# Optimization experiments

Hardware: AMD Instinct MI355X
Metric: run time of the kernel (lower is better)

The kernel has to match this reference:

```python
import jax, jax.numpy as jnp
import numpy as np

N, E, DIN, H, DOUT, G = 100000, 1600000, 32, 64, 8, 64
NUM_PROC = 2
EDGE_DIM = 15


def setup_inputs() -> dict:
    key = jax.random.key(0)
    ks = jax.random.split(key, 20)
    s = 0.1
    return {
        "x": jax.random.normal(ks[0], (N, DIN), dtype=jnp.float32),
        "edge_index": jax.random.randint(ks[1], (2, E), 0, N, dtype=jnp.int32),
        "edge_attr": jax.random.normal(ks[2], (E, EDGE_DIM), dtype=jnp.float32),
        "batch": jnp.sort(jax.random.randint(ks[3], (N,), 0, G, dtype=jnp.int32)),
        "enc_W": jax.random.normal(ks[4], (DIN, H)) * s,
        "enc_b": jnp.zeros((H,), jnp.float32),
        "lin_W": jax.random.normal(ks[5], (NUM_PROC, H, H)) * s,
        "lin_b": jnp.zeros((NUM_PROC, H), jnp.float32),
        "edge_W": jax.random.normal(ks[6], (NUM_PROC, EDGE_DIM, H)) * s,
        "edge_b": jnp.zeros((NUM_PROC, H), jnp.float32),
        "att_W1": jax.random.normal(ks[7], (H, H // 2)) * s,
        "att_b1": jnp.zeros((H // 2,), jnp.float32),
        "att_W2": jax.random.normal(ks[8], (H // 2, 1)) * s,
        "att_b2": jnp.zeros((1,), jnp.float32),
        "dec_W1": jax.random.normal(ks[9], (H, H // 2)) * s,
        "dec_b1": jnp.zeros((H // 2,), jnp.float32),
        "dec_W2": jax.random.normal(ks[10], (H // 2, DOUT)) * s,
        "dec_b2": jnp.zeros((DOUT,), jnp.float32),
    }


def reference(x, edge_index, edge_attr, batch, enc_W, enc_b, lin_W, lin_b,
              edge_W, edge_b, att_W1, att_b1, att_W2, att_b2,
              dec_W1, dec_b1, dec_W2, dec_b2):
    src, dst = edge_index[0], edge_index[1]
    n = x.shape[0]
    # encoder
    h = jax.nn.relu(x @ enc_W + enc_b)
    # message passing layers: gather x_j -> linear + edge embedding -> scatter-add
    for l in range(NUM_PROC):
        msg = h[src] @ lin_W[l] + lin_b[l] + edge_attr @ edge_W[l] + edge_b[l]  # [E, H]
        h = jax.nn.relu(jax.ops.segment_sum(msg, dst, num_segments=n))
    # attention global pooling: segment softmax over graphs in `batch`
    scores = (jax.nn.relu(h @ att_W1 + att_b1) @ att_W2 + att_b2)[:, 0]  # [N]
    m = jax.ops.segment_max(scores, batch, num_segments=G)
    e = jnp.exp(scores - m[batch])
    denom = jax.ops.segment_sum(e, batch, num_segments=G)
    attn = e / denom[batch]
    g = jax.ops.segment_sum(h * attn[:, None], batch, num_segments=G)  # [G, H]
    # decoder
    return jax.nn.relu(g @ dec_W1 + dec_b1) @ dec_W2 + dec_b2
```

## Files before the change

### kernel.cpp

```cpp
#include <hip/hip_runtime.h>

#define DIN 32
#define HDIM 64
#define DOUT 8
#define NGRAPH 64
#define EDIM 15
#define SCAN_BS 512

__device__ __forceinline__ int clampidx(int v, int n) {
    return ((unsigned)v < (unsigned)n) ? v : 0;
}

__device__ __forceinline__ unsigned short f2b(float f) {
    unsigned int u = __float_as_uint(f);
    u = (u + 0x7FFF + ((u >> 16) & 1)) >> 16;
    return (unsigned short)u;
}
__device__ __forceinline__ float b2f(unsigned short b) {
    return __uint_as_float(((unsigned int)b) << 16);
}

__device__ __forceinline__ unsigned int fkey(float f) {
    unsigned int b = __float_as_uint(f);
    return (b & 0x80000000u) ? ~b : (b | 0x80000000u);
}
__device__ __forceinline__ float funkey(unsigned int k) {
    unsigned int b = (k & 0x80000000u) ? (k ^ 0x80000000u) : ~k;
    return __uint_as_float(b);
}

__global__ __launch_bounds__(256) void k_enc_b(const float* __restrict__ x,
                                               const float* __restrict__ W,
                                               const float* __restrict__ b,
                                               unsigned short* __restrict__ h, int n_nodes) {
    __shared__ float xs[4][DIN];
    const int j = threadIdx.x & 63;
    const int q = threadIdx.x >> 6;
    const int n = blockIdx.x * 4 + q;
    const bool ok = (n < n_nodes);
    if (ok && j < DIN) xs[q][j] = x[(size_t)n * DIN + j];
    __syncthreads();
    if (ok) {
        float acc = b[j];
#pragma unroll
        for (int k = 0; k < DIN; ++k) acc = fmaf(xs[q][k], W[k * HDIM + j], acc);
        h[(size_t)n * HDIM + j] = f2b(fmaxf(acc, 0.f));
    }
}

__global__ __launch_bounds__(256) void k_ecvt(const float* __restrict__ eattr,
                                              unsigned short* __restrict__ eb, int E) {
    size_t i = (size_t)blockIdx.x * blockDim.x + threadIdx.x;
    const size_t stride = (size_t)gridDim.x * blockDim.x;
    const size_t total = (size_t)E * 16;
    for (; i < total; i += stride) {
        int d = (int)(i & 15);
        size_t e = i >> 4;
        eb[i] = (d < EDIM) ? f2b(eattr[e * EDIM + d]) : 0;
    }
}

__global__ __launch_bounds__(256) void k_deg(const int* __restrict__ ei,
                                             int* __restrict__ degi,
                                             int* __restrict__ rank, int E, int n_nodes) {
    int e = blockIdx.x * blockDim.x + threadIdx.x;
    if (e < E) rank[e] = atomicAdd(&degi[clampidx(ei[E + e], n_nodes)], 1);
}

__global__ __launch_bounds__(SCAN_BS) void k_blocksum(const int* __restrict__ degi,
                                                      int* __restrict__ bsum, int n) {
    __shared__ int red[SCAN_BS];
    const int t = threadIdx.x;
    const int i = blockIdx.x * SCAN_BS + t;
    red[t] = (i < n) ? degi[i] : 0;
    __syncthreads();
    for (int off = SCAN_BS / 2; off >= 1; off >>= 1) {
        if (t < off) red[t] += red[t + off];
        __syncthreads();
    }
    if (t == 0) bsum[blockIdx.x] = red[0];
}

__global__ __launch_bounds__(64) void k_bscan(const int* __restrict__ bsum,
                                              int* __restrict__ boff,
                                              int* __restrict__ offsets,
                                              int nblk, int n, int E) {
    if (blockIdx.x == 0 && threadIdx.x == 0) {
        int run = 0;
        for (int b = 0; b < nblk; ++b) { boff[b] = run; run += bsum[b]; }
        offsets[n] = E;
    }
}

__global__ __launch_bounds__(64) void k_fillofs(const int* __restrict__ degi,
                                                const int* __restrict__ boff,
                                                int* __restrict__ offsets, int n) {
    if (threadIdx.x != 0) return;
    const int b = blockIdx.x;
    int run = boff[b];
    const int i0 = b * SCAN_BS;
    const int i1 = (i0 + SCAN_BS < n) ? i0 + SCAN_BS : n;
    for (int i = i0; i < i1; ++i) {
        offsets[i] = run;
        run += degi[i];
    }
}

__global__ __launch_bounds__(256) void k_fill(const int* __restrict__ ei,
                                              const int* __restrict__ offsets,
                                              const int* __restrict__ rank,
                                              int2* __restrict__ pe, int E, int n_nodes) {
    int e = blockIdx.x * blockDim.x + threadIdx.x;
    if (e >= E) return;
    int dst = clampidx(ei[E + e], n_nodes);
    int pos = offsets[dst] + rank[e];
    if ((unsigned)pos < (unsigned)E) pe[pos] = make_int2(clampidx(ei[e], n_nodes), e);
}

__global__ __launch_bounds__(256) void k_gxf0(const unsigned short* __restrict__ hprev,
                                              const unsigned short* __restrict__ eb,
                                              const int* __restrict__ degi,
                                              const int* __restrict__ offsets,
                                              const int2* __restrict__ pe,
                                              const float* __restrict__ linW,
                                              const float* __restrict__ linb,
                                              const float* __restrict__ edgeW,
                                              const float* __restrict__ edgeb,
                                              unsigned short* __restrict__ hnext,
                                              float* __restrict__ ea_out,
                                              int n_nodes, int E) {
    __shared__ float As[4][HDIM];
    __shared__ float es[4][EDIM];
    const int j = threadIdx.x & 63;
    const int q = threadIdx.x >> 6;
    const bool ed = (j < EDIM);
    int w  = (blockIdx.x * blockDim.x + threadIdx.x) >> 6;
    const int nw = (gridDim.x * blockDim.x) >> 6;
    for (int n = w; n < n_nodes; n += nw) {
        int rs = offsets[n], re = offsets[n + 1];
        if (rs < 0) rs = 0;
        if (re > E) re = E;
        if (re < rs) re = rs;
        float A0 = 0.f, A1 = 0.f, A2 = 0.f, A3 = 0.f;
        float e0 = 0.f, e1 = 0.f, e2 = 0.f, e3 = 0.f;
        int jj = rs;
        for (; jj + 4 <= re; jj += 4) {
            int2 p0 = pe[jj], p1 = pe[jj + 1], p2 = pe[jj + 2], p3 = pe[jj + 3];
            int s0 = clampidx(p0.x, n_nodes), s1 = clampidx(p1.x, n_nodes);
            int s2 = clampidx(p2.x, n_nodes), s3 = clampidx(p3.x, n_nodes);
            A0 += b2f(hprev[(size_t)s0 * HDIM + j]);
            A1 += b2f(hprev[(size_t)s1 * HDIM + j]);
            A2 += b2f(hprev[(size_t)s2 * HDIM + j]);
            A3 += b2f(hprev[(size_t)s3 * HDIM + j]);
            if (ed) {
                e0 += b2f(eb[(size_t)clampidx(p0.y, E) * 16 + j]);
                e1 += b2f(eb[(size_t)clampidx(p1.y, E) * 16 + j]);
                e2 += b2f(eb[(size_t)clampidx(p2.y, E) * 16 + j]);
                e3 += b2f(eb[(size_t)clampidx(p3.y, E) * 16 + j]);
            }
        }
        for (; jj < re; ++jj) {
            int2 p = pe[jj];
            A0 += b2f(hprev[(size_t)clampidx(p.x, n_nodes) * HDIM + j]);
            if (ed) e0 += b2f(eb[(size_t)clampidx(p.y, E) * 16 + j]);
        }
        As[q][j] = (A0 + A1) + (A2 + A3);
        float eacc = (e0 + e1) + (e2 + e3);
        if (ed) {
            es[q][j] = eacc;
            ea_out[(size_t)n * 16 + j] = eacc;
        }
        __builtin_amdgcn_wave_barrier();
        float acc = (linb[j] + edgeb[j]) * (float)degi[n];
#pragma unroll
        for (int k = 0; k < HDIM; ++k) acc = fmaf(As[q][k], linW[k * HDIM + j], acc);
#pragma unroll
        for (int k = 0; k < EDIM; ++k) acc = fmaf(es[q][k], edgeW[k * HDIM + j], acc);
        hnext[(size_t)n * HDIM + j] = f2b(fmaxf(acc, 0.f));
    }
}

__global__ __launch_bounds__(256) void k_gxf1(const unsigned short* __restrict__ hprev,
                                              const float* __restrict__ ea,
                                              const int* __restrict__ degi,
                                              const int* __restrict__ offsets,
                                              const int2* __restrict__ pe,
                                              const float* __restrict__ linW,
                                              const float* __restrict__ linb,
                                              const float* __restrict__ edgeW,
                                              const float* __restrict__ edgeb,
                                              float* __restrict__ hnext, int n_nodes, int E) {
    __shared__ float As[4][HDIM];
    __shared__ float es[4][EDIM];
    const int j = threadIdx.x & 63;
    const int q = threadIdx.x >> 6;
    int w  = (blockIdx.x * blockDim.x + threadIdx.x) >> 6;
    const int nw = (gridDim.x * blockDim.x) >> 6;
    for (int n = w; n < n_nodes; n += nw) {
        int rs = offsets[n], re = offsets[n + 1];
        if (rs < 0) rs = 0;
        if (re > E) re = E;
        if (re < rs) re = rs;
        float A0 = 0.f, A1 = 0.f, A2 = 0.f, A3 = 0.f;
        int jj = rs;
        for (; jj + 4 <= re; jj += 4) {
            int s0 = clampidx(pe[jj].x,     n_nodes);
            int s1 = clampidx(pe[jj + 1].x, n_nodes);
            int s2 = clampidx(pe[jj + 2].x, n_nodes);
            int s3 = clampidx(pe[jj + 3].x, n_nodes);
            A0 += b2f(hprev[(size_t)s0 * HDIM + j]);
            A1 += b2f(hprev[(size_t)s1 * HDIM + j]);
            A2 += b2f(hprev[(size_t)s2 * HDIM + j]);
            A3 += b2f(hprev[(size_t)s3 * HDIM + j]);
        }
        for (; jj < re; ++jj) A0 += b2f(hprev[(size_t)clampidx(pe[jj].x, n_nodes) * HDIM + j]);
        As[q][j] = (A0 + A1) + (A2 + A3);
        if (j < EDIM) es[q][j] = ea[(size_t)n * 16 + j];
        __builtin_amdgcn_wave_barrier();
        float acc = (linb[j] + edgeb[j]) * (float)degi[n];
#pragma unroll
        for (int k = 0; k < HDIM; ++k) acc = fmaf(As[q][k], linW[k * HDIM + j], acc);
#pragma unroll
        for (int k = 0; k < EDIM; ++k) acc = fmaf(es[q][k], edgeW[k * HDIM + j], acc);
        hnext[(size_t)n * HDIM + j] = fmaxf(acc, 0.f);
    }
}

__global__ __launch_bounds__(256) void k_sc_b(const float* __restrict__ h,
                                              const float* __restrict__ W1,
                                              const float* __restrict__ b1,
                                              const float* __restrict__ W2,
                                              const float* __restrict__ b2,
                                              float* __restrict__ s, int n_nodes) {
    __shared__ float hs[4][HDIM];
    const int j = threadIdx.x & 63;
    const int q = threadIdx.x >> 6;
    const int n = blockIdx.x * 4 + q;
    const bool ok = (n < n_nodes);
    if (ok) hs[q][j] = h[(size_t)n * HDIM + j];
    __builtin_amdgcn_wave_barrier();
    float t = 0.f;
    if (ok && j < 32) {
        float z = b1[j];
#pragma unroll
        for (int k = 0; k < HDIM; ++k) z = fmaf(hs[q][k], W1[k * 32 + j], z);
        t = fmaxf(z, 0.f) * W2[j];
    }
    t += __shfl_xor(t, 1, 64);
    t += __shfl_xor(t, 2, 64);
    t += __shfl_xor(t, 4, 64);
    t += __shfl_xor(t, 8, 64);
    t += __shfl_xor(t, 16, 64);
    if (ok && j == 0) s[n] = t + b2[0];
}

__global__ __launch_bounds__(256) void k_poolA(const float* __restrict__ s,
                                               const int* __restrict__ batch,
                                               unsigned int* __restrict__ gmaxi, int n_nodes) {
    const int gi = blockIdx.x >> 3;
    const int c  = blockIdx.x & 7;
    __shared__ int se[2];
    __shared__ float red[256];
    if (threadIdx.x == 0) {
        int lo = 0, hi = n_nodes;
        while (lo < hi) { int mid = (lo + hi) >> 1; if (batch[mid] < gi) lo = mid + 1; else hi = mid; }
        se[0] = lo;
        lo = 0; hi = n_nodes;
        while (lo < hi) { int mid = (lo + hi) >> 1; if (batch[mid] < gi + 1) lo = mid + 1; else hi = mid; }
        se[1] = lo;
    }
    __syncthreads();
    const int start = se[0], len = se[1] - se[0];
    const int cs = start + (int)(((long long)len * c) >> 3);
    const int ce = start + (int)(((long long)len * (c + 1)) >> 3);
    float mx = -3.4e38f;
    for (int i = cs + threadIdx.x; i < ce; i += 256) mx = fmaxf(mx, s[i]);
    red[threadIdx.x] = mx;
    __syncthreads();
    for (int off = 128; off >= 1; off >>= 1) {
        if (threadIdx.x < off) red[threadIdx.x] = fmaxf(red[threadIdx.x], red[threadIdx.x + off]);
        __syncthreads();
    }
    if (threadIdx.x == 0 && ce > cs) atomicMax(&gmaxi[gi], fkey(red[0]));
}

__global__ __launch_bounds__(256) void k_poolB(const float* __restrict__ s,
                                               const float* __restrict__ h,
                                               const int* __restrict__ batch,
                                               const unsigned int* __restrict__ gmaxi,
                                               float* __restrict__ gden,
                                               float* __restrict__ gacc, int n_nodes) {
    const int gi = blockIdx.x >> 3;
    const int c  = blockIdx.x & 7;
    __shared__ int se[2];
    __shared__ float ws[256];
    __shared__ float redd[256];
    if (threadIdx.x == 0) {
        int lo = 0, hi = n_nodes;
        while (lo < hi) { int mid = (lo + hi) >> 1; if (batch[mid] < gi) lo = mid + 1; else hi = mid; }
        se[0] = lo;
        lo = 0; hi = n_nodes;
        while (lo < hi) { int mid = (lo + hi) >> 1; if (batch[mid] < gi + 1) lo = mid + 1; else hi = mid; }
        se[1] = lo;
    }
    __syncthreads();
    const int start = se[0], len = se[1] - se[0];
    const int cs = start + (int)(((long long)len * c) >> 3);
    const int ce = start + (int)(((long long)len * (c + 1)) >> 3);
    const float m = funkey(gmaxi[gi]);
    const int tid = threadIdx.x, d = tid & 63, q = tid >> 6;
    float den = 0.f, acc = 0.f;
    for (int t0 = cs; t0 < ce; t0 += 256) {
        const int cnt = (ce - t0 < 256) ? (ce - t0) : 256;
        __syncthreads();
        if (tid < cnt) {
            float wv = __expf(s[t0 + tid] - m);
            ws[tid] = wv;
            den += wv;
        }
        __syncthreads();
        for (int i = q; i < cnt; i += 4)
            acc = fmaf(h[(size_t)(t0 + i) * HDIM + d], ws[i], acc);
    }
    redd[tid] = den;
    __syncthreads();
    for (int off = 128; off >= 1; off >>= 1) {
        if (tid < off) redd[tid] += redd[tid + off];
        __syncthreads();
    }
    if (tid == 0 && redd[0] != 0.f) atomicAdd(&gden[gi], redd[0]);
    if (acc != 0.f) atomicAdd(&gacc[gi * HDIM + d], acc);
}

__global__ __launch_bounds__(64) void k_dec_b(const float* __restrict__ gacc,
                                              const float* __restrict__ gden,
                                              const float* __restrict__ W1,
                                              const float* __restrict__ b1,
                                              const float* __restrict__ W2,
                                              const float* __restrict__ b2,
                                              float* __restrict__ out) {
    __shared__ float gg[HDIM];
    __shared__ float zs[32];
    const int gi = blockIdx.x;
    const int j = threadIdx.x;
    const float den = gden[gi];
    gg[j] = (den > 0.f) ? gacc[gi * HDIM + j] / den : 0.f;
    __syncthreads();
    if (j < 32) {
        float z = b1[j];
#pragma unroll
        for (int k = 0; k < HDIM; ++k) z = fmaf(gg[k], W1[k * 32 + j], z);
        zs[j] = fmaxf(z, 0.f);
    }
    __syncthreads();
    if (j < DOUT) {
        float o = b2[j];
#pragma unroll
        for (int i = 0; i < 32; ++i) o = fmaf(zs[i], W2[i * DOUT + j], o);
        out[gi * DOUT + j] = o;
    }
}

extern "C" void kernel_launch(void* const* d_in, const int* in_sizes, int n_in,
                              void* d_out, int out_size, void* d_ws, size_t ws_size,
                              hipStream_t stream) {
    const float* x     = (const float*)d_in[0];
    const int*   ei    = (const int*)d_in[1];
    const float* eattr = (const float*)d_in[2];
    const int*   batch = (const int*)d_in[3];
    const float* encW  = (const float*)d_in[4];
    const float* encb  = (const float*)d_in[5];
    const float* linW  = (const float*)d_in[6];
    const float* linb  = (const float*)d_in[7];
    const float* edgeW = (const float*)d_in[8];
    const float* edgeb = (const float*)d_in[9];
    const float* attW1 = (const float*)d_in[10];
    const float* attb1 = (const float*)d_in[11];
    const float* attW2 = (const float*)d_in[12];
    const float* attb2 = (const float*)d_in[13];
    const float* decW1 = (const float*)d_in[14];
    const float* decb1 = (const float*)d_in[15];
    const float* decW2 = (const float*)d_in[16];
    const float* decb2 = (const float*)d_in[17];

    const int N = in_sizes[0] / DIN;
    const int E = in_sizes[1] / 2;
    const int nblk = (N + SCAN_BS - 1) / SCAN_BS;

    size_t union_bytes = (size_t)E * 16 * 2;
    size_t b2_bytes = (size_t)N * HDIM * 4;
    if (b2_bytes > union_bytes) union_bytes = b2_bytes;

    size_t need_bytes = union_bytes
                      + (size_t)N * HDIM * 2 * 2
                      + (size_t)N * 16 * 4
                      + (size_t)N * 4
                      + (size_t)NGRAPH * (HDIM + 2) * 4
                      + (size_t)E * 8
                      + (size_t)N * 4
                      + (size_t)(N + 2) * 4
                      + (size_t)E * 4
                      + 8192 * 4;
    if (ws_size < need_bytes) {
        return;
    }

    char* base = (char*)d_ws;
    float* B2 = (float*)base;
    unsigned short* eb = (unsigned short*)base;
    unsigned short* hb0 = (unsigned short*)(base + union_bytes);
    unsigned short* hb1 = hb0 + (size_t)N * HDIM;
    float* ea = (float*)(hb1 + (size_t)N * HDIM);
    float* sS = ea + (size_t)N * 16;
    float* gacc = sS + N;
    float* gden = gacc + NGRAPH * HDIM;
    unsigned int* gmaxi = (unsigned int*)(gden + NGRAPH);
    int2* pe     = (int2*)(gmaxi + NGRAPH);
    int* degi    = (int*)(pe + E);
    int* offsets = degi + N;
    int* rank    = offsets + (N + 2);
    int* bsum    = rank + E;
    int* boff    = bsum + 4096;

    hipMemsetAsync(degi, 0, (size_t)N * sizeof(int), stream);
    hipMemsetAsync(gacc, 0, (size_t)NGRAPH * (HDIM + 2) * sizeof(float), stream);

    k_enc_b<<<(N + 3) / 4, 256, 0, stream>>>(x, encW, encb, hb0, N);
    k_ecvt<<<4096, 256, 0, stream>>>(eattr, eb, E);
    k_deg<<<(E + 255) / 256, 256, 0, stream>>>(ei, degi, rank, E, N);

    k_blocksum<<<nblk, SCAN_BS, 0, stream>>>(degi, bsum, N);
    k_bscan<<<1, 64, 0, stream>>>(bsum, boff, offsets, nblk, N, E);
    k_fillofs<<<nblk, 64, 0, stream>>>(degi, boff, offsets, N);
    k_fill<<<(E + 255) / 256, 256, 0, stream>>>(ei, offsets, rank, pe, E, N);

    k_gxf0<<<2048, 256, 0, stream>>>(hb0, eb, degi, offsets, pe,
                                     linW, linb, edgeW, edgeb, hb1, ea, N, E);

    k_gxf1<<<2048, 256, 0, stream>>>(hb1, ea, degi, offsets, pe,
                                     linW + HDIM * HDIM, linb + HDIM,
                                     edgeW + EDIM * HDIM, edgeb + HDIM, B2, N, E);

    k_sc_b<<<(N + 3) / 4, 256, 0, stream>>>(B2, attW1, attb1, attW2, attb2, sS, N);
    k_poolA<<<NGRAPH * 8, 256, 0, stream>>>(sS, batch, gmaxi, N);
    k_poolB<<<NGRAPH * 8, 256, 0, stream>>>(sS, B2, batch, gmaxi, gden, gacc, N);
    k_dec_b<<<NGRAPH, 64, 0, stream>>>(gacc, gden, decW1, decb1, decW2, decb2, (float*)d_out);
}
```

Baseline: 594.6 us.

## Permute edge attributes into CSR order during fill; fuse score and max pooling

The edge-attribute bf16 conversion moves into the CSR fill kernel and writes directly at each edge's sorted position. The message-passing gather then reads edge attributes contiguously instead of through a random edge index, and the pair array shrinks to a plain source list. Separately, the attention-score kernel is fused with the per-graph max reduction, which removes one launch and one pass over the scores. The fill kernel now scatters 32-byte rows to random positions, and the fused score kernel uses only 512 blocks, which may reduce parallelism.

```diff
diff --git a/kernel.cpp b/kernel.cpp
--- a/kernel.cpp
+++ b/kernel.cpp
@@ -45,18 +45,6 @@
 #pragma unroll
         for (int k = 0; k < DIN; ++k) acc = fmaf(xs[q][k], W[k * HDIM + j], acc);
         h[(size_t)n * HDIM + j] = f2b(fmaxf(acc, 0.f));
-    }
-}
-
-__global__ __launch_bounds__(256) void k_ecvt(const float* __restrict__ eattr,
-                                              unsigned short* __restrict__ eb, int E) {
-    size_t i = (size_t)blockIdx.x * blockDim.x + threadIdx.x;
-    const size_t stride = (size_t)gridDim.x * blockDim.x;
-    const size_t total = (size_t)E * 16;
-    for (; i < total; i += stride) {
-        int d = (int)(i & 15);
-        size_t e = i >> 4;
-        eb[i] = (d < EDIM) ? f2b(eattr[e * EDIM + d]) : 0;
     }
 }
 
@@ -106,22 +94,36 @@
     }
 }
 
-__global__ __launch_bounds__(256) void k_fill(const int* __restrict__ ei,
-                                              const int* __restrict__ offsets,
-                                              const int* __restrict__ rank,
-                                              int2* __restrict__ pe, int E, int n_nodes) {
-    int e = blockIdx.x * blockDim.x + threadIdx.x;
-    if (e >= E) return;
-    int dst = clampidx(ei[E + e], n_nodes);
-    int pos = offsets[dst] + rank[e];
-    if ((unsigned)pos < (unsigned)E) pe[pos] = make_int2(clampidx(ei[e], n_nodes), e);
+__global__ __launch_bounds__(256) void k_fillx(const int* __restrict__ ei,
+                                               const int* __restrict__ offsets,
+                                               const int* __restrict__ rank,
+                                               const float* __restrict__ eattr,
+                                               int* __restrict__ srcl,
+                                               unsigned short* __restrict__ eb,
+                                               int E, int n_nodes) {
+    const int lane = threadIdx.x & 63;
+    const int grp  = lane >> 4;
+    const int d    = lane & 15;
+    int w  = (blockIdx.x * blockDim.x + threadIdx.x) >> 6;
+    const int nw = (gridDim.x * blockDim.x) >> 6;
+    const int ngroups = (E + 3) >> 2;
+    for (int eg = w; eg < ngroups; eg += nw) {
+        int e = eg * 4 + grp;
+        if (e >= E) continue;
+        int dst = clampidx(ei[E + e], n_nodes);
+        int pos = offsets[dst] + rank[e];
+        if ((unsigned)pos < (unsigned)E) {
+            if (d == 0) srcl[pos] = clampidx(ei[e], n_nodes);
+            if (d < EDIM) eb[(size_t)pos * 16 + d] = f2b(eattr[(size_t)e * EDIM + d]);
+        }
+    }
 }
 
 __global__ __launch_bounds__(256) void k_gxf0(const unsigned short* __restrict__ hprev,
                                               const unsigned short* __restrict__ eb,
                                               const int* __restrict__ degi,
                                               const int* __restrict__ offsets,
-                                              const int2* __restrict__ pe,
+                                              const int* __restrict__ srcl,
                                               const float* __restrict__ linW,
                                               const float* __restrict__ linb,
                                               const float* __restrict__ edgeW,
@@ -145,24 +147,24 @@
         float e0 = 0.f, e1 = 0.f, e2 = 0.f, e3 = 0.f;
         int jj = rs;
         for (; jj + 4 <= re; jj += 4) {
-            int2 p0 = pe[jj], p1 = pe[jj + 1], p2 = pe[jj + 2], p3 = pe[jj + 3];
-            int s0 = clampidx(p0.x, n_nodes), s1 = clampidx(p1.x, n_nodes);
-            int s2 = clampidx(p2.x, n_nodes), s3 = clampidx(p3.x, n_nodes);
+            int s0 = clampidx(srcl[jj],     n_nodes);
+            int s1 = clampidx(srcl[jj + 1], n_nodes);
+            int s2 = clampidx(srcl[jj + 2], n_nodes);
+            int s3 = clampidx(srcl[jj + 3], n_nodes);
             A0 += b2f(hprev[(size_t)s0 * HDIM + j]);
             A1 += b2f(hprev[(size_t)s1 * HDIM + j]);
             A2 += b2f(hprev[(size_t)s2 * HDIM + j]);
             A3 += b2f(hprev[(size_t)s3 * HDIM + j]);
             if (ed) {
-                e0 += b2f(eb[(size_t)clampidx(p0.y, E) * 16 + j]);
-                e1 += b2f(eb[(size_t)clampidx(p1.y, E) * 16 + j]);
-                e2 += b2f(eb[(size_t)clampidx(p2.y, E) * 16 + j]);
-                e3 += b2f(eb[(size_t)clampidx(p3.y, E) * 16 + j]);
+                e0 += b2f(eb[(size_t)jj * 16 + j]);
+                e1 += b2f(eb[(size_t)(jj + 1) * 16 + j]);
+                e2 += b2f(eb[(size_t)(jj + 2) * 16 + j]);
+                e3 += b2f(eb[(size_t)(jj + 3) * 16 + j]);
             }
         }
         for (; jj < re; ++jj) {
-            int2 p = pe[jj];
-            A0 += b2f(hprev[(size_t)clampidx(p.x, n_nodes) * HDIM + j]);
-            if (ed) e0 += b2f(eb[(size_t)clampidx(p.y, E) * 16 + j]);
+            A0 += b2f(hprev[(size_t)clampidx(srcl[jj], n_nodes) * HDIM + j]);
+            if (ed) e0 += b2f(eb[(size_t)jj * 16 + j]);
         }
         As[q][j] = (A0 + A1) + (A2 + A3);
         float eacc = (e0 + e1) + (e2 + e3);
@@ -184,7 +186,7 @@
                                               const float* __restrict__ ea,
                                               const int* __restrict__ degi,
                                               const int* __restrict__ offsets,
-                                              const int2* __restrict__ pe,
+                                              const int* __restrict__ srcl,
                                               const float* __restrict__ linW,
                                               const float* __restrict__ linb,
                                               const float* __restrict__ edgeW,
@@ -204,16 +206,16 @@
         float A0 = 0.f, A1 = 0.f, A2 = 0.f, A3 = 0.f;
         int jj = rs;
         for (; jj + 4 <= re; jj += 4) {
-            int s0 = clampidx(pe[jj].x,     n_nodes);
-            int s1 = clampidx(pe[jj + 1].x, n_nodes);
-            int s2 = clampidx(pe[jj + 2].x, n_nodes);
-            int s3 = clampidx(pe[jj + 3].x, n_nodes);
+            int s0 = clampidx(srcl[jj],     n_nodes);
+            int s1 = clampidx(srcl[jj + 1], n_nodes);
+            int s2 = clampidx(srcl[jj + 2], n_nodes);
+            int s3 = clampidx(srcl[jj + 3], n_nodes);
             A0 += b2f(hprev[(size_t)s0 * HDIM + j]);
             A1 += b2f(hprev[(size_t)s1 * HDIM + j]);
             A2 += b2f(hprev[(size_t)s2 * HDIM + j]);
             A3 += b2f(hprev[(size_t)s3 * HDIM + j]);
         }
-        for (; jj < re; ++jj) A0 += b2f(hprev[(size_t)clampidx(pe[jj].x, n_nodes) * HDIM + j]);
+        for (; jj < re; ++jj) A0 += b2f(hprev[(size_t)clampidx(srcl[jj], n_nodes) * HDIM + j]);
         As[q][j] = (A0 + A1) + (A2 + A3);
         if (j < EDIM) es[q][j] = ea[(size_t)n * 16 + j];
         __builtin_amdgcn_wave_barrier();
@@ -226,41 +228,19 @@
     }
 }
 
-__global__ __launch_bounds__(256) void k_sc_b(const float* __restrict__ h,
-                                              const float* __restrict__ W1,
-                                              const float* __restrict__ b1,
-                                              const float* __restrict__ W2,
-                                              const float* __restrict__ b2,
-                                              float* __restrict__ s, int n_nodes) {
-    __shared__ float hs[4][HDIM];
-    const int j = threadIdx.x & 63;
-    const int q = threadIdx.x >> 6;
-    const int n = blockIdx.x * 4 + q;
-    const bool ok = (n < n_nodes);
-    if (ok) hs[q][j] = h[(size_t)n * HDIM + j];
-    __builtin_amdgcn_wave_barrier();
-    float t = 0.f;
-    if (ok && j < 32) {
-        float z = b1[j];
-#pragma unroll
-        for (int k = 0; k < HDIM; ++k) z = fmaf(hs[q][k], W1[k * 32 + j], z);
-        t = fmaxf(z, 0.f) * W2[j];
-    }
-    t += __shfl_xor(t, 1, 64);
-    t += __shfl_xor(t, 2, 64);
-    t += __shfl_xor(t, 4, 64);
-    t += __shfl_xor(t, 8, 64);
-    t += __shfl_xor(t, 16, 64);
-    if (ok && j == 0) s[n] = t + b2[0];
-}
-
-__global__ __launch_bounds__(256) void k_poolA(const float* __restrict__ s,
-                                               const int* __restrict__ batch,
-                                               unsigned int* __restrict__ gmaxi, int n_nodes) {
+__global__ __launch_bounds__(256) void k_pscore(const float* __restrict__ h,
+                                                const int* __restrict__ batch,
+                                                const float* __restrict__ W1,
+                                                const float* __restrict__ b1,
+                                                const float* __restrict__ W2,
+                                                const float* __restrict__ b2,
+                                                float* __restrict__ s,
+                                                unsigned int* __restrict__ gmaxi, int n_nodes) {
     const int gi = blockIdx.x >> 3;
     const int c  = blockIdx.x & 7;
     __shared__ int se[2];
-    __shared__ float red[256];
+    __shared__ float hs[4][HDIM];
+    __shared__ float redm[4];
     if (threadIdx.x == 0) {
         int lo = 0, hi = n_nodes;
         while (lo < hi) { int mid = (lo + hi) >> 1; if (batch[mid] < gi) lo = mid + 1; else hi = mid; }
@@ -273,15 +253,38 @@
     const int start = se[0], len = se[1] - se[0];
     const int cs = start + (int)(((long long)len * c) >> 3);
     const int ce = start + (int)(((long long)len * (c + 1)) >> 3);
+    const int j = threadIdx.x & 63;
+    const int q = threadIdx.x >> 6;
+    const float b2v = b2[0];
     float mx = -3.4e38f;
-    for (int i = cs + threadIdx.x; i < ce; i += 256) mx = fmaxf(mx, s[i]);
-    red[threadIdx.x] = mx;
-    __syncthreads();
-    for (int off = 128; off >= 1; off >>= 1) {
-        if (threadIdx.x < off) red[threadIdx.x] = fmaxf(red[threadIdx.x], red[threadIdx.x + off]);
-        __syncthreads();
-    }
-    if (threadIdx.x == 0 && ce > cs) atomicMax(&gmaxi[gi], fkey(red[0]));
+    for (int i = cs + q; i < ce; i += 4) {
+        hs[q][j] = h[(size_t)i * HDIM + j];
+        __builtin_amdgcn_wave_barrier();
+        float t = 0.f;
+        if (j < 32) {
+            float z = b1[j];
+#pragma unroll
+            for (int k = 0; k < HDIM; ++k) z = fmaf(hs[q][k], W1[k * 32 + j], z);
+            t = fmaxf(z, 0.f) * W2[j];
+        }
+        t += __shfl_xor(t, 1, 64);
+        t += __shfl_xor(t, 2, 64);
+        t += __shfl_xor(t, 4, 64);
+        t += __shfl_xor(t, 8, 64);
+        t += __shfl_xor(t, 16, 64);
+        if (j == 0) {
+            float sv = t + b2v;
+            s[i] = sv;
+            mx = fmaxf(mx, sv);
+        }
+        __builtin_amdgcn_wave_barrier();
+    }
+    if (j == 0) redm[q] = mx;
+    __syncthreads();
+    if (threadIdx.x == 0 && ce > cs) {
+        float m = fmaxf(fmaxf(redm[0], redm[1]), fmaxf(redm[2], redm[3]));
+        atomicMax(&gmaxi[gi], fkey(m));
+    }
 }
 
 __global__ __launch_bounds__(256) void k_poolB(const float* __restrict__ s,
@@ -396,7 +399,7 @@
                       + (size_t)N * 16 * 4
                       + (size_t)N * 4
                       + (size_t)NGRAPH * (HDIM + 2) * 4
-                      + (size_t)E * 8
+                      + (size_t)E * 4
                       + (size_t)N * 4
                       + (size_t)(N + 2) * 4
                       + (size_t)E * 4
@@ -415,8 +418,8 @@
     float* gacc = sS + N;
     float* gden = gacc + NGRAPH * HDIM;
     unsigned int* gmaxi = (unsigned int*)(gden + NGRAPH);
-    int2* pe     = (int2*)(gmaxi + NGRAPH);
-    int* degi    = (int*)(pe + E);
+    int* srcl    = (int*)(gmaxi + NGRAPH);
+    int* degi    = srcl + E;
     int* offsets = degi + N;
     int* rank    = offsets + (N + 2);
     int* bsum    = rank + E;
@@ -426,23 +429,23 @@
     hipMemsetAsync(gacc, 0, (size_t)NGRAPH * (HDIM + 2) * sizeof(float), stream);
 
     k_enc_b<<<(N + 3) / 4, 256, 0, stream>>>(x, encW, encb, hb0, N);
-    k_ecvt<<<4096, 256, 0, stream>>>(eattr, eb, E);
     k_deg<<<(E + 255) / 256, 256, 0, stream>>>(ei, degi, rank, E, N);
 
     k_blocksum<<<nblk, SCAN_BS, 0, stream>>>(degi, bsum, N);
     k_bscan<<<1, 64, 0, stream>>>(bsum, boff, offsets, nblk, N, E);
     k_fillofs<<<nblk, 64, 0, stream>>>(degi, boff, offsets, N);
-    k_fill<<<(E + 255) / 256, 256, 0, stream>>>(ei, offsets, rank, pe, E, N);
-
-    k_gxf0<<<2048, 256, 0, stream>>>(hb0, eb, degi, offsets, pe,
+
+    k_fillx<<<2048, 256, 0, stream>>>(ei, offsets, rank, eattr, srcl, eb, E, N);
+
+    k_gxf0<<<2048, 256, 0, stream>>>(hb0, eb, degi, offsets, srcl,
                                      linW, linb, edgeW, edgeb, hb1, ea, N, E);
 
-    k_gxf1<<<2048, 256, 0, stream>>>(hb1, ea, degi, offsets, pe,
+    k_gxf1<<<2048, 256, 0, stream>>>(hb1, ea, degi, offsets, srcl,
                                      linW + HDIM * HDIM, linb + HDIM,
                                      edgeW + EDIM * HDIM, edgeb + HDIM, B2, N, E);
 
-    k_sc_b<<<(N + 3) / 4, 256, 0, stream>>>(B2, attW1, attb1, attW2, attb2, sS, N);
-    k_poolA<<<NGRAPH * 8, 256, 0, stream>>>(sS, batch, gmaxi, N);
+    k_pscore<<<NGRAPH * 8, 256, 0, stream>>>(B2, batch, attW1, attb1, attW2, attb2,
+                                             sS, gmaxi, N);
     k_poolB<<<NGRAPH * 8, 256, 0, stream>>>(sS, B2, batch, gmaxi, gden, gacc, N);
     k_dec_b<<<NGRAPH, 64, 0, stream>>>(gacc, gden, decW1, decb1, decW2, decb2, (float*)d_out);
 }
```

Measured after the change: 594.2 us. About the same (-0.1%).
